# Optimization experiments

Measured on AMD Instinct MI355X. Metric: run time of the kernel, lower is better.

Reference implementation:

```python
import jax, jax.numpy as jnp
import numpy as np

B, T, C, NH = 4, 2048, 1024, 16
D = C // NH  # 64


def setup_inputs() -> dict:
    key = jax.random.key(0)
    ks = jax.random.split(key, 6)
    x = jax.random.normal(ks[0], (B, T, C), dtype=jnp.float32)
    # realistic RoPE tables: interleaved cos/sin over T positions, D head dim
    inv_freq = 1.0 / (10000.0 ** (np.arange(0, D, 2, dtype=np.float32) / D))
    ang = np.arange(T, dtype=np.float32)[:, None] * inv_freq[None, :]  # (T, D/2)
    ang = np.repeat(ang, 2, axis=-1)  # (T, D) interleaved
    pe_cos = jnp.asarray(np.cos(ang))[None, None]  # (1,1,T,D)
    pe_sin = jnp.asarray(np.sin(ang))[None, None]
    pe_scale = jax.random.uniform(ks[1], (1, 1, T, D), dtype=jnp.float32, minval=0.5, maxval=1.5)
    mask = 0.1 * jax.random.normal(ks[2], (1, B, T, T), dtype=jnp.float32)
    w_qkv = jax.random.normal(ks[3], (3 * C, C), dtype=jnp.float32) * (C ** -0.5)
    b_qkv = jax.random.normal(ks[4], (3 * C,), dtype=jnp.float32) * 0.02
    return {"x": x, "pe_cos": pe_cos, "pe_sin": pe_sin, "pe_scale": pe_scale,
            "mask": mask, "w_qkv": w_qkv, "b_qkv": b_qkv}


def _rotate_interleaved(u):
    # even positions <- -odd, odd positions <- even (RoPE interleave)
    u2 = u.reshape(u.shape[:-1] + (-1, 2))
    rot = jnp.stack([-u2[..., 1], u2[..., 0]], axis=-1)
    return rot.reshape(u.shape)


def reference(x, pe_cos, pe_sin, pe_scale, mask, w_qkv, b_qkv):
    b, t, c = x.shape
    qkv = x @ w_qkv.T + b_qkv  # (b, t, 3c)
    q, k, v = jnp.split(qkv, 3, axis=-1)
    # (b, t, nh, d) -> (b, nh, t, d)
    to_heads = lambda u: u.reshape(b, t, NH, D).transpose(0, 2, 1, 3)
    q, k, v = to_heads(q), to_heads(k), to_heads(v)
    # pe tensors (1,1,t,d) broadcast over (b,nh,t,d)
    q = (q * pe_cos + _rotate_interleaved(q) * pe_sin) * pe_scale
    k = (k * pe_cos + _rotate_interleaved(k) * pe_sin) / pe_scale
    scale = 1.0 / ((2.0 * D) ** 0.5)  # original uses scale=1/sqrt(2d)
    scores = jnp.einsum('bhqd,bhkd->bhqk', q, k) * scale
    # torch layout was (nh, b, t, t) + mask (1, b, t, t): mask broadcasts over heads
    scores = scores + jnp.swapaxes(mask, 0, 1)  # mask -> (b, 1, t, t)
    attn = jax.nn.softmax(scores, axis=-1)
    out = jnp.einsum('bhqk,bhkd->bhqd', attn, v)  # (b, nh, t, d)
    return out.transpose(0, 2, 1, 3).reshape(b, t, c)
```

## Files before the change

### kernel.cpp

```cpp
#include <hip/hip_runtime.h>
#include <math.h>

#define NB 4
#define NT 2048
#define NC 1024
#define NHEADS 16
#define HDIM 64

typedef __attribute__((ext_vector_type(8))) _Float16 half8v;
typedef __attribute__((ext_vector_type(4))) float f32x4;

__device__ inline unsigned short f2h(float f) {
    _Float16 h = (_Float16)f;
    return __builtin_bit_cast(unsigned short, h);
}
__device__ inline float h2f(unsigned short u) {
    return (float)__builtin_bit_cast(_Float16, u);
}

#define AS1C(p) ((const __attribute__((address_space(1))) unsigned int*)(unsigned long long)(const void*)(p))
#define AS3P(p) ((__attribute__((address_space(3))) unsigned int*)(unsigned int)(unsigned long long)(void*)(p))
#define GLL16(gp, lp) __builtin_amdgcn_global_load_lds(AS1C(gp), AS3P(lp), 16, 0, 0)

__global__ __launch_bounds__(256) void conv_f16_kernel(
    const float* __restrict__ in, unsigned short* __restrict__ out, int n4)
{
    const int i = blockIdx.x * 256 + threadIdx.x;
    if (i >= n4) return;
    const float4 f = ((const float4*)in)[i];
    ushort4 h;
    h.x = f2h(f.x); h.y = f2h(f.y); h.z = f2h(f.z); h.w = f2h(f.w);
    ((ushort4*)out)[i] = h;
}

__global__ __launch_bounds__(256) void mask_conv_kernel(
    const float* __restrict__ in, unsigned short* __restrict__ out)
{
    const size_t i = (size_t)blockIdx.x * 256 + threadIdx.x;
    const int row = (int)(i >> 9);
    const int c4 = (int)(i & 511);
    const int ktb = c4 >> 4;
    const int fr = c4 & 15;
    const float* ip = in + (size_t)row * NT + ktb * 64 + fr;
    ushort4 o;
    o.x = f2h(ip[0]);
    o.y = f2h(ip[16]);
    o.z = f2h(ip[32]);
    o.w = f2h(ip[48]);
    ((ushort4*)out)[i] = o;
}

__global__ __launch_bounds__(256) void qkv_gemm_kernel(
    const unsigned short* __restrict__ xf, const unsigned short* __restrict__ wf,
    const float* __restrict__ bias, const float* __restrict__ pe_cos,
    const float* __restrict__ pe_sin, const float* __restrict__ pe_scale,
    unsigned short* __restrict__ qb, unsigned short* __restrict__ kb,
    unsigned short* __restrict__ vtb)
{
    __shared__ __align__(16) unsigned short Ah[128 * 32];
    __shared__ __align__(16) unsigned short Bh[128 * 32];

    const int tid = threadIdx.x;
    const int w = tid >> 6, lane = tid & 63;
    const int g = lane >> 4, fr = lane & 15;
    const int wr = w >> 1, wc = w & 1;

    const int bid = blockIdx.x;
    const int s = (bid & 7) * 192 + (bid >> 3);
    const int m0 = (s & 63) * 128, n0 = (s >> 6) * 128;

    const int c0 = tid, c1 = tid + 256;
    const int r0 = c0 >> 2, r1 = c1 >> 2;
    const int cb0 = ((c0 & 3) * 16) ^ (((r0 >> 1) & 3) << 4);
    const int cb1 = ((c1 & 3) * 16) ^ (((r1 >> 1) & 3) << 4);
    const unsigned short* px0 = xf + (size_t)(m0 + r0) * NC + (cb0 >> 1);
    const unsigned short* px1 = xf + (size_t)(m0 + r1) * NC + (cb1 >> 1);
    const unsigned short* pw0 = wf + (size_t)(n0 + r0) * NC + (cb0 >> 1);
    const unsigned short* pw1 = wf + (size_t)(n0 + r1) * NC + (cb1 >> 1);

    f32x4 acc[4][4];
#pragma unroll
    for (int m = 0; m < 4; ++m)
#pragma unroll
        for (int n = 0; n < 4; ++n) acc[m][n] = (f32x4){0.f, 0.f, 0.f, 0.f};

    for (int k0 = 0; k0 < NC; k0 += 32) {
        __syncthreads();
        GLL16(px0 + k0, (char*)Ah + c0 * 16);
        GLL16(px1 + k0, (char*)Ah + c1 * 16);
        GLL16(pw0 + k0, (char*)Bh + c0 * 16);
        GLL16(pw1 + k0, (char*)Bh + c1 * 16);
        __syncthreads();

        half8v a_f[4], b_f[4];
#pragma unroll
        for (int m = 0; m < 4; ++m) {
            const int r = wr * 64 + m * 16 + fr;
            const int off = r * 64 + ((g * 16) ^ (((r >> 1) & 3) << 4));
            a_f[m] = *(const half8v*)((const char*)Ah + off);
        }
#pragma unroll
        for (int n = 0; n < 4; ++n) {
            const int r = wc * 64 + n * 16 + fr;
            const int off = r * 64 + ((g * 16) ^ (((r >> 1) & 3) << 4));
            b_f[n] = *(const half8v*)((const char*)Bh + off);
        }
#pragma unroll
        for (int m = 0; m < 4; ++m)
#pragma unroll
            for (int n = 0; n < 4; ++n)
                acc[m][n] = __builtin_amdgcn_mfma_f32_16x16x32_f16(a_f[m], b_f[n], acc[m][n], 0, 0, 0);
    }

#pragma unroll
    for (int n = 0; n < 4; ++n) {
        const int col = n0 + wc * 64 + n * 16 + fr;
        const int part = col >> 10;
        const int hh = (col & 1023) >> 6;
        const int dd = col & 63;
        const float bv = bias[col];
#pragma unroll
        for (int m = 0; m < 4; ++m) {
            const int row0 = m0 + wr * 64 + m * 16 + 4 * g;
            const int bb = row0 >> 11;
            const int t0 = row0 & 2047;
            if (part < 2) {
                unsigned short* outp = (part == 0) ? qb : kb;
#pragma unroll
                for (int j = 0; j < 4; ++j) {
                    const int t = t0 + j;
                    float val = acc[m][n][j] + bv;
                    const float partner = __shfl_xor(val, 1, 64);
                    const int pidx = t * HDIM + dd;
                    const float cc = pe_cos[pidx], ss = pe_sin[pidx], sc = pe_scale[pidx];
                    const float r = (dd & 1) ? (val * cc + partner * ss)
                                             : (val * cc - partner * ss);
                    val = (part == 0) ? (r * sc) : (r / sc);
                    outp[(((size_t)bb * NHEADS + hh) * NT + t) * HDIM + dd] = f2h(val);
                }
            } else {
                ushort4 sv;
                sv.x = f2h(acc[m][n][0] + bv);
                sv.y = f2h(acc[m][n][1] + bv);
                sv.z = f2h(acc[m][n][2] + bv);
                sv.w = f2h(acc[m][n][3] + bv);
                *(ushort4*)&vtb[(((size_t)bb * NHEADS + hh) * HDIM + dd) * NT + t0] = sv;
            }
        }
    }
}

__global__ __launch_bounds__(256) void attn_mfma_kernel(
    const unsigned short* __restrict__ qb, const unsigned short* __restrict__ kb,
    const unsigned short* __restrict__ vtb, const unsigned short* __restrict__ m16,
    float* __restrict__ out)
{
    __shared__ __align__(16) unsigned short Ks[2][64 * 64];
    __shared__ __align__(16) unsigned short Vs[2][64 * 64];
    __shared__ __align__(16) unsigned short Ps[4][32 * 64];

    const int tid = threadIdx.x;
    const int w = tid >> 6, lane = tid & 63;
    const int g = lane >> 4, fr = lane & 15;

    const int bid = blockIdx.x;
    const int s = (bid & 7) * 128 + (bid >> 3);
    const int q0 = (s & 15) * 128;
    const int h = (s >> 4) & 15;
    const int b = s >> 8;

    const size_t bh = (size_t)b * NHEADS + h;
    const unsigned short* qp = qb + (bh * NT + q0 + w * 32) * HDIM;
    const unsigned short* kp = kb + bh * NT * HDIM;
    const unsigned short* vtp = vtb + bh * HDIM * NT;
    const unsigned short* mp = m16 + ((size_t)b * NT + q0 + w * 32) * NT;

    const int sc0 = tid, sc1 = tid + 256;
    const int sr0 = sc0 >> 3, scb0 = ((sc0 & 7) * 16) ^ ((sr0 & 7) << 4);
    const int sr1 = sc1 >> 3, scb1 = ((sc1 & 7) * 16) ^ ((sr1 & 7) << 4);

#define STAGE(buf, kt)                                                          \
    do {                                                                        \
        const unsigned short* ktp_ = kp + (kt) * 64 * HDIM;                     \
        GLL16(ktp_ + sr0 * HDIM + (scb0 >> 1), (char*)Ks[buf] + sc0 * 16);      \
        GLL16(vtp + (size_t)sr0 * NT + (kt) * 64 + (scb0 >> 1),                 \
              (char*)Vs[buf] + sc0 * 16);                                       \
        GLL16(ktp_ + sr1 * HDIM + (scb1 >> 1), (char*)Ks[buf] + sc1 * 16);      \
        GLL16(vtp + (size_t)sr1 * NT + (kt) * 64 + (scb1 >> 1),                 \
              (char*)Vs[buf] + sc1 * 16);                                       \
    } while (0)

    half8v qf[2][2];
#pragma unroll
    for (int m = 0; m < 2; ++m)
#pragma unroll
        for (int kk = 0; kk < 2; ++kk)
            qf[m][kk] = *(const half8v*)(qp + (m * 16 + fr) * HDIM + kk * 32 + g * 8);

    f32x4 acc[2][4];
    float li[2][4], mi[2][4];
#pragma unroll
    for (int m = 0; m < 2; ++m)
#pragma unroll
        for (int j = 0; j < 4; ++j) {
            li[m][j] = 0.f; mi[m][j] = -3.0e38f;
            acc[m][j] = (f32x4){0.f, 0.f, 0.f, 0.f};
        }
    const float scl = 0.08838834764831845f;

    STAGE(0, 0);
    __syncthreads();
    int cur = 0;

    for (int kt = 0; kt < NT / 64; ++kt) {
        if (kt + 1 < NT / 64) STAGE(cur ^ 1, kt + 1);

        half8v kf[4][2];
#pragma unroll
        for (int nt = 0; nt < 4; ++nt) {
            const int r = nt * 16 + fr;
#pragma unroll
            for (int kk = 0; kk < 2; ++kk) {
                const int off = r * 128 + ((kk * 64 + g * 16) ^ ((r & 7) << 4));
                kf[nt][kk] = *(const half8v*)((const char*)Ks[cur] + off);
            }
        }

#pragma unroll
        for (int m = 0; m < 2; ++m) {
            f32x4 Sm[4];
#pragma unroll
            for (int nt = 0; nt < 4; ++nt) {
                Sm[nt] = (f32x4){0.f, 0.f, 0.f, 0.f};
#pragma unroll
                for (int kk = 0; kk < 2; ++kk)
                    Sm[nt] = __builtin_amdgcn_mfma_f32_16x16x32_f16(qf[m][kk], kf[nt][kk], Sm[nt], 0, 0, 0);
            }

            float sv[4][4], rmj[4];
#pragma unroll
            for (int j = 0; j < 4; ++j) {
                const ushort4 mv = *(const ushort4*)(
                    mp + (size_t)(m * 16 + 4 * g + j) * NT + kt * 64 + fr * 4);
                sv[j][0] = fmaf(Sm[0][j], scl, h2f(mv.x));
                sv[j][1] = fmaf(Sm[1][j], scl, h2f(mv.y));
                sv[j][2] = fmaf(Sm[2][j], scl, h2f(mv.z));
                sv[j][3] = fmaf(Sm[3][j], scl, h2f(mv.w));
                rmj[j] = fmaxf(fmaxf(sv[j][0], sv[j][1]), fmaxf(sv[j][2], sv[j][3]));
            }

            const float worst = fmaxf(fmaxf(rmj[0] - mi[m][0], rmj[1] - mi[m][1]),
                                      fmaxf(rmj[2] - mi[m][2], rmj[3] - mi[m][3]));
            if (!__all(worst <= 8.f)) {
#pragma unroll
                for (int j = 0; j < 4; ++j) {
                    float rm = rmj[j];
                    rm = fmaxf(rm, __shfl_xor(rm, 1, 64));
                    rm = fmaxf(rm, __shfl_xor(rm, 2, 64));
                    rm = fmaxf(rm, __shfl_xor(rm, 4, 64));
                    rm = fmaxf(rm, __shfl_xor(rm, 8, 64));
                    const float mnew = fmaxf(mi[m][j], rm);
                    const float alpha = __expf(mi[m][j] - mnew);
                    li[m][j] *= alpha;
#pragma unroll
                    for (int dt = 0; dt < 4; ++dt) acc[m][dt][j] *= alpha;
                    mi[m][j] = mnew;
                }
            }

#pragma unroll
            for (int j = 0; j < 4; ++j) {
                const int prow = m * 16 + 4 * g + j;
                float ps = 0.f;
#pragma unroll
                for (int nt = 0; nt < 4; ++nt) {
                    const float p = __expf(sv[j][nt] - mi[m][j]);
                    const int off = prow * 128 + ((nt * 32 + fr * 2) ^ ((prow & 7) << 4));
                    *(unsigned short*)((char*)Ps[w] + off) = f2h(p);
                    ps += p;
                }
                li[m][j] += ps;
            }
        }

        half8v vf[4][2];
#pragma unroll
        for (int dt = 0; dt < 4; ++dt) {
            const int d = dt * 16 + fr;
#pragma unroll
            for (int kk = 0; kk < 2; ++kk) {
                const int off = d * 128 + ((kk * 64 + g * 16) ^ ((d & 7) << 4));
                vf[dt][kk] = *(const half8v*)((const char*)Vs[cur] + off);
            }
        }
#pragma unroll
        for (int m = 0; m < 2; ++m) {
            half8v pf[2];
#pragma unroll
            for (int kk = 0; kk < 2; ++kk) {
                const int off = (m * 16 + fr) * 128 + ((kk * 64 + g * 16) ^ ((fr & 7) << 4));
                pf[kk] = *(const half8v*)((const char*)Ps[w] + off);
            }
#pragma unroll
            for (int dt = 0; dt < 4; ++dt)
#pragma unroll
                for (int kk = 0; kk < 2; ++kk)
                    acc[m][dt] = __builtin_amdgcn_mfma_f32_16x16x32_f16(pf[kk], vf[dt][kk], acc[m][dt], 0, 0, 0);
        }

        __syncthreads();
        cur ^= 1;
    }

#pragma unroll
    for (int m = 0; m < 2; ++m)
#pragma unroll
        for (int j = 0; j < 4; ++j) {
            float lt = li[m][j];
            lt += __shfl_xor(lt, 1, 64);
            lt += __shfl_xor(lt, 2, 64);
            lt += __shfl_xor(lt, 4, 64);
            lt += __shfl_xor(lt, 8, 64);
            const float inv = 1.f / lt;
            const int t = q0 + w * 32 + m * 16 + 4 * g + j;
            float* op = out + (((size_t)b * NT + t) * NHEADS + h) * HDIM;
#pragma unroll
            for (int dt = 0; dt < 4; ++dt) op[dt * 16 + fr] = acc[m][dt][j] * inv;
        }
}

extern "C" void kernel_launch(void* const* d_in, const int* in_sizes, int n_in,
                              void* d_out, int out_size, void* d_ws, size_t ws_size,
                              hipStream_t stream) {
    const float* x        = (const float*)d_in[0];
    const float* pe_cos   = (const float*)d_in[1];
    const float* pe_sin   = (const float*)d_in[2];
    const float* pe_scale = (const float*)d_in[3];
    const float* mask     = (const float*)d_in[4];
    const float* w_qkv    = (const float*)d_in[5];
    const float* b_qkv    = (const float*)d_in[6];
    float* out = (float*)d_out;

    unsigned short* ws = (unsigned short*)d_ws;
    const size_t PER = (size_t)NB * NHEADS * NT * HDIM;
    unsigned short* qbuf = ws;
    unsigned short* kbuf = ws + PER;
    unsigned short* vtbuf = ws + 2 * PER;
    unsigned short* xbuf = ws + 3 * PER;
    unsigned short* wbuf = xbuf + (size_t)NB * NT * NC;
    unsigned short* maskbuf = ws + 3 * PER;

    conv_f16_kernel<<<8192, 256, 0, stream>>>(x, xbuf, (NB * NT * NC) / 4);
    conv_f16_kernel<<<3072, 256, 0, stream>>>(w_qkv, wbuf, (3 * NC * NC) / 4);
    qkv_gemm_kernel<<<1536, 256, 0, stream>>>(xbuf, wbuf, b_qkv,
                                              pe_cos, pe_sin, pe_scale,
                                              qbuf, kbuf, vtbuf);
    mask_conv_kernel<<<16384, 256, 0, stream>>>(mask, maskbuf);
    attn_mfma_kernel<<<1024, 256, 0, stream>>>(qbuf, kbuf, vtbuf, maskbuf, out);
}
```

Measured before the change: 260.6 us.

## Fold softmax scale into Q, use exp2, and permute key order for packed P stores

Folds the 1/sqrt(2d) scale and log2(e) into Q in the QKV epilogue and pre-multiplies the fp16 mask by log2(e), so the attention loop drops the per-score FMA scale and uses the hardware exp2 instead of expf. Within each 64-key tile, keys are permuted consistently in the mask, the stored V^T and the P tile. Each lane can then write its four P values as one packed 8-byte LDS store via cvt_pkrtz, instead of four scalar 2-byte stores. The risks are the extra rounding from folding scales into fp16 Q and the mask, and the reliance on the permutation matching across all three buffers.

```diff
diff --git a/kernel.cpp b/kernel.cpp
--- a/kernel.cpp
+++ b/kernel.cpp
@@ -8,7 +8,11 @@
 #define HDIM 64
 
 typedef __attribute__((ext_vector_type(8))) _Float16 half8v;
+typedef __attribute__((ext_vector_type(4))) _Float16 half4v;
+typedef __attribute__((ext_vector_type(2))) __fp16 fp16x2;
 typedef __attribute__((ext_vector_type(4))) float f32x4;
+
+#define LOG2E 1.4426950408889634f
 
 __device__ inline unsigned short f2h(float f) {
     _Float16 h = (_Float16)f;
@@ -16,6 +20,17 @@
 }
 __device__ inline float h2f(unsigned short u) {
     return (float)__builtin_bit_cast(_Float16, u);
+}
+__device__ inline float exp2fast(float x) {
+#if __has_builtin(__builtin_amdgcn_exp2f)
+    return __builtin_amdgcn_exp2f(x);
+#else
+    return exp2f(x);
+#endif
+}
+__device__ inline unsigned int pack2h(float a, float b) {
+    fp16x2 p = __builtin_amdgcn_cvt_pkrtz(a, b);
+    return __builtin_bit_cast(unsigned int, p);
 }
 
 #define AS1C(p) ((const __attribute__((address_space(1))) unsigned int*)(unsigned long long)(const void*)(p))
@@ -43,10 +58,10 @@
     const int fr = c4 & 15;
     const float* ip = in + (size_t)row * NT + ktb * 64 + fr;
     ushort4 o;
-    o.x = f2h(ip[0]);
-    o.y = f2h(ip[16]);
-    o.z = f2h(ip[32]);
-    o.w = f2h(ip[48]);
+    o.x = f2h(ip[0] * LOG2E);
+    o.y = f2h(ip[16] * LOG2E);
+    o.z = f2h(ip[32] * LOG2E);
+    o.w = f2h(ip[48] * LOG2E);
     ((ushort4*)out)[i] = o;
 }
 
@@ -112,6 +127,7 @@
                 acc[m][n] = __builtin_amdgcn_mfma_f32_16x16x32_f16(a_f[m], b_f[n], acc[m][n], 0, 0, 0);
     }
 
+    const float QSCL = 0.08838834764831845f * LOG2E;
 #pragma unroll
     for (int n = 0; n < 4; ++n) {
         const int col = n0 + wc * 64 + n * 16 + fr;
@@ -119,13 +135,13 @@
         const int hh = (col & 1023) >> 6;
         const int dd = col & 63;
         const float bv = bias[col];
-#pragma unroll
-        for (int m = 0; m < 4; ++m) {
-            const int row0 = m0 + wr * 64 + m * 16 + 4 * g;
-            const int bb = row0 >> 11;
-            const int t0 = row0 & 2047;
-            if (part < 2) {
-                unsigned short* outp = (part == 0) ? qb : kb;
+        if (part < 2) {
+            unsigned short* outp = (part == 0) ? qb : kb;
+#pragma unroll
+            for (int m = 0; m < 4; ++m) {
+                const int row0 = m0 + wr * 64 + m * 16 + 4 * g;
+                const int bb = row0 >> 11;
+                const int t0 = row0 & 2047;
 #pragma unroll
                 for (int j = 0; j < 4; ++j) {
                     const int t = t0 + j;
@@ -135,16 +151,24 @@
                     const float cc = pe_cos[pidx], ss = pe_sin[pidx], sc = pe_scale[pidx];
                     const float r = (dd & 1) ? (val * cc + partner * ss)
                                              : (val * cc - partner * ss);
-                    val = (part == 0) ? (r * sc) : (r / sc);
+                    val = (part == 0) ? (r * sc * QSCL) : (r / sc);
                     outp[(((size_t)bb * NHEADS + hh) * NT + t) * HDIM + dd] = f2h(val);
                 }
-            } else {
+            }
+        } else {
+            const int rowb = m0 + wr * 64;
+            const int bb = rowb >> 11;
+            const int tb = rowb & 2047;
+            unsigned short* vp2 =
+                &vtb[(((size_t)bb * NHEADS + hh) * HDIM + dd) * NT + tb];
+#pragma unroll
+            for (int j = 0; j < 4; ++j) {
                 ushort4 sv;
-                sv.x = f2h(acc[m][n][0] + bv);
-                sv.y = f2h(acc[m][n][1] + bv);
-                sv.z = f2h(acc[m][n][2] + bv);
-                sv.w = f2h(acc[m][n][3] + bv);
-                *(ushort4*)&vtb[(((size_t)bb * NHEADS + hh) * HDIM + dd) * NT + t0] = sv;
+                sv.x = f2h(acc[0][n][j] + bv);
+                sv.y = f2h(acc[1][n][j] + bv);
+                sv.z = f2h(acc[2][n][j] + bv);
+                sv.w = f2h(acc[3][n][j] + bv);
+                *(ushort4*)&vp2[(4 * g + j) * 4] = sv;
             }
         }
     }
@@ -206,7 +230,7 @@
             li[m][j] = 0.f; mi[m][j] = -3.0e38f;
             acc[m][j] = (f32x4){0.f, 0.f, 0.f, 0.f};
         }
-    const float scl = 0.08838834764831845f;
+    const float THR = 11.541560327111708f;
 
     STAGE(0, 0);
     __syncthreads();
@@ -242,16 +266,16 @@
             for (int j = 0; j < 4; ++j) {
                 const ushort4 mv = *(const ushort4*)(
                     mp + (size_t)(m * 16 + 4 * g + j) * NT + kt * 64 + fr * 4);
-                sv[j][0] = fmaf(Sm[0][j], scl, h2f(mv.x));
-                sv[j][1] = fmaf(Sm[1][j], scl, h2f(mv.y));
-                sv[j][2] = fmaf(Sm[2][j], scl, h2f(mv.z));
-                sv[j][3] = fmaf(Sm[3][j], scl, h2f(mv.w));
+                sv[j][0] = Sm[0][j] + h2f(mv.x);
+                sv[j][1] = Sm[1][j] + h2f(mv.y);
+                sv[j][2] = Sm[2][j] + h2f(mv.z);
+                sv[j][3] = Sm[3][j] + h2f(mv.w);
                 rmj[j] = fmaxf(fmaxf(sv[j][0], sv[j][1]), fmaxf(sv[j][2], sv[j][3]));
             }
 
             const float worst = fmaxf(fmaxf(rmj[0] - mi[m][0], rmj[1] - mi[m][1]),
                                       fmaxf(rmj[2] - mi[m][2], rmj[3] - mi[m][3]));
-            if (!__all(worst <= 8.f)) {
+            if (!__all(worst <= THR)) {
 #pragma unroll
                 for (int j = 0; j < 4; ++j) {
                     float rm = rmj[j];
@@ -260,7 +284,7 @@
                     rm = fmaxf(rm, __shfl_xor(rm, 4, 64));
                     rm = fmaxf(rm, __shfl_xor(rm, 8, 64));
                     const float mnew = fmaxf(mi[m][j], rm);
-                    const float alpha = __expf(mi[m][j] - mnew);
+                    const float alpha = exp2fast(mi[m][j] - mnew);
                     li[m][j] *= alpha;
 #pragma unroll
                     for (int dt = 0; dt < 4; ++dt) acc[m][dt][j] *= alpha;
@@ -271,15 +295,16 @@
 #pragma unroll
             for (int j = 0; j < 4; ++j) {
                 const int prow = m * 16 + 4 * g + j;
-                float ps = 0.f;
-#pragma unroll
-                for (int nt = 0; nt < 4; ++nt) {
-                    const float p = __expf(sv[j][nt] - mi[m][j]);
-                    const int off = prow * 128 + ((nt * 32 + fr * 2) ^ ((prow & 7) << 4));
-                    *(unsigned short*)((char*)Ps[w] + off) = f2h(p);
-                    ps += p;
-                }
-                li[m][j] += ps;
+                const float p0 = exp2fast(sv[j][0] - mi[m][j]);
+                const float p1 = exp2fast(sv[j][1] - mi[m][j]);
+                const float p2 = exp2fast(sv[j][2] - mi[m][j]);
+                const float p3 = exp2fast(sv[j][3] - mi[m][j]);
+                li[m][j] += (p0 + p1) + (p2 + p3);
+                uint2 pw2;
+                pw2.x = pack2h(p0, p1);
+                pw2.y = pack2h(p2, p3);
+                const int off = prow * 128 + ((fr * 8) ^ ((prow & 7) << 4));
+                *(uint2*)((char*)Ps[w] + off) = pw2;
             }
         }
 
```

Result: faster. 254.8 us (-2.2%).
